# Performance work log

Hardware: AMD Instinct MI355X
Metric: run time of the kernel (lower is better)

## Reference

```python
import jax, jax.numpy as jnp
import numpy as np

NUM_HEADS = 8
OUTPUT_DIM = 64  # per-head dim
TEMP = float(OUTPUT_DIM ** 0.5)  # torch code: 1 / output_dim ** (-0.5) == sqrt(output_dim)


def setup_inputs() -> dict:
    key = jax.random.key(0)
    ks = jax.random.split(key, 5)
    B, N, Lq, S, D = 8, 4, 64, 1024, 1024
    inner = OUTPUT_DIM * NUM_HEADS  # 512
    scale = 0.02
    return {
        "q": jax.random.normal(ks[0], (B, N, Lq, D), dtype=jnp.float32),
        "k_v": jax.random.normal(ks[1], (B, N, S, D), dtype=jnp.float32),
        "W_kv": jax.random.normal(ks[2], (inner * 2, D), dtype=jnp.float32) * scale,
        "W_q": jax.random.normal(ks[3], (inner, D), dtype=jnp.float32) * scale,
        "W_out": jax.random.normal(ks[4], (D, inner), dtype=jnp.float32) * scale,
    }


def _split_heads(x):
    # b n s (h d) -> b n h s d
    b, n, s, hd = x.shape
    return x.reshape(b, n, s, NUM_HEADS, hd // NUM_HEADS).transpose(0, 1, 3, 2, 4)


def reference(q, k_v, W_kv, W_q, W_out):
    # Concatenate latents onto the key/value sequence (Perceiver resampler style)
    kv = jnp.concatenate([k_v, q], axis=-2)            # [b, n, S+Lq, D]
    k, v = jnp.split(kv @ W_kv.T, 2, axis=-1)          # each [b, n, S+Lq, h*d]
    qp = q @ W_q.T                                     # [b, n, Lq, h*d]
    qh = _split_heads(qp) * TEMP                       # NOTE: up-scaled by sqrt(d), as in source
    kh = _split_heads(k)
    vh = _split_heads(v)
    scores = jnp.einsum('bnhqd,bnhkd->bnhqk', qh, kh)
    attn = jax.nn.softmax(scores, axis=-1)
    o = jnp.einsum('bnhqk,bnhkd->bnhqd', attn, vh)
    b, n, h, s, d = o.shape
    o = o.transpose(0, 1, 3, 2, 4).reshape(b, n, s, h * d)  # b n h s d -> b n s (h d)
    return o @ W_out.T
```

## Files before the change

kernel.cpp:

```cpp
#include <hip/hip_runtime.h>
#include <math.h>


namespace {

typedef __attribute__((ext_vector_type(8))) short s16x8;
typedef __attribute__((ext_vector_type(4))) float f32x4;

constexpr int LDP = 68;
constexpr int LDB = 72;

constexpr size_t CWS_OFF  = 0;
constexpr size_t QP_OFF   = 142606336;
constexpr size_t WKVH_OFF = 146800640;
constexpr size_t WKVL_OFF = 148897792;
constexpr size_t WQH_OFF  = 150994944;
constexpr size_t WQL_OFF  = 152043520;
constexpr size_t WOH_OFF  = 153092096;
constexpr size_t WOL_OFF  = 154140672;
constexpr size_t OHI_OFF  = 155189248;
constexpr size_t OLO_OFF  = 157286400;
constexpr size_t WS_REQUIRED = 159383552;

__device__ __forceinline__ float4 ld4(const float* p) {
    return *reinterpret_cast<const float4*>(p);
}
__device__ __forceinline__ unsigned short f2bf(float x) {
    unsigned u = __float_as_uint(x);
    u += 0x7fffu + ((u >> 16) & 1u);
    return (unsigned short)(u >> 16);
}
__device__ __forceinline__ float bf2f(unsigned short h) {
    return __uint_as_float(((unsigned)h) << 16);
}
__device__ __forceinline__ f32x4 mfma16(s16x8 a, s16x8 b, f32x4 c) {
    return __builtin_amdgcn_mfma_f32_16x16x32_bf16(a, b, c, 0, 0, 0);
}

__device__ __forceinline__ void cvt_row(const float* __restrict__ src,
                                        unsigned short* __restrict__ dhi,
                                        unsigned short* __restrict__ dlo, int nelem) {
    const int t = threadIdx.x;
    if (t * 4 < nelem) {
        float4 v = ld4(src + t * 4);
        ushort4 hi, lo;
        hi.x = f2bf(v.x); lo.x = f2bf(v.x - bf2f(hi.x));
        hi.y = f2bf(v.y); lo.y = f2bf(v.y - bf2f(hi.y));
        hi.z = f2bf(v.z); lo.z = f2bf(v.z - bf2f(hi.z));
        hi.w = f2bf(v.w); lo.w = f2bf(v.w - bf2f(hi.w));
        *reinterpret_cast<ushort4*>(dhi + t * 4) = hi;
        *reinterpret_cast<ushort4*>(dlo + t * 4) = lo;
    }
}

__device__ __forceinline__ unsigned packbf(float x) {
    const unsigned short h = f2bf(x);
    return ((unsigned)h << 16) | (unsigned)f2bf(x - bf2f(h));
}

__global__ __launch_bounds__(256)
void cvt_b(float* __restrict__ kv, float* __restrict__ q,
           const float* __restrict__ Wkv, const float* __restrict__ Wq,
           const float* __restrict__ Wout,
           unsigned short* Wkvh, unsigned short* Wkvl,
           unsigned short* Wqh, unsigned short* Wql,
           unsigned short* Woh, unsigned short* Wol)
{
    const int b = blockIdx.x;
    const int t = threadIdx.x;
    if (b < 34816) {
        const int bn = b / 1088, s = b % 1088;
        float* row = (s < 1024) ? kv + ((size_t)bn * 1024 + s) * 1024
                                : q  + ((size_t)bn * 64 + (s - 1024)) * 1024;
        float4 v = ld4(row + t * 4);
        uint4 p;
        p.x = packbf(v.x); p.y = packbf(v.y);
        p.z = packbf(v.z); p.w = packbf(v.w);
        *reinterpret_cast<uint4*>(row + t * 4) = p;
    } else if (b < 34816 + 1024) {
        const int r = b - 34816;
        cvt_row(Wkv + (size_t)r * 1024, Wkvh + (size_t)r * 1024, Wkvl + (size_t)r * 1024, 1024);
    } else if (b < 34816 + 1536) {
        const int r = b - 34816 - 1024;
        cvt_row(Wq + (size_t)r * 1024, Wqh + (size_t)r * 1024, Wql + (size_t)r * 1024, 1024);
    } else {
        const int r = b - 34816 - 1536;
        cvt_row(Wout + (size_t)r * 512, Woh + (size_t)r * 512, Wol + (size_t)r * 512, 512);
    }
}

template<int CONCAT>
__global__ __launch_bounds__(256, 2)
void gemm_packed(const unsigned* __restrict__ Akv, const unsigned* __restrict__ Aq,
                 const unsigned short* __restrict__ Bhi, const unsigned short* __restrict__ Blo,
                 float* __restrict__ C, int N, int K, float scale)
{
    __shared__ short Ah[128][LDB], Al[128][LDB], Bh[128][LDB], Bl[128][LDB];

    const int bm   = blockIdx.y, bnn = blockIdx.x;
    const int tid  = threadIdx.x;
    const int lane = tid & 63, wave = tid >> 6;
    const int wr   = wave >> 1, wc = wave & 1;
    const int fr   = lane & 15, kg = lane >> 4;

    const unsigned* abase[8];
    int aprow[8], apcol[8];
    #pragma unroll
    for (int s2 = 0; s2 < 8; ++s2) {
        const int u = tid + 256 * s2;
        aprow[s2] = u >> 4;
        apcol[s2] = (u & 15) * 4;
        const int R = bm * 128 + aprow[s2];
        if (CONCAT) {
            const int bn = R / 1088, s = R - bn * 1088;
            abase[s2] = (s < 1024) ? Akv + ((size_t)bn * 1024 + s) * (size_t)K
                                   : Aq  + ((size_t)bn * 64 + (s - 1024)) * (size_t)K;
        } else {
            abase[s2] = Akv + (size_t)R * (size_t)K;
        }
    }
    int brow[4], bkk[4];
    #pragma unroll
    for (int s2 = 0; s2 < 4; ++s2) {
        const int u = tid + 256 * s2;
        brow[s2] = u >> 3;
        bkk[s2]  = (u & 7) * 8;
    }

    f32x4 acc[4][4] = {};

    for (int kc = 0; kc < K; kc += 64) {
        uint4 pa[8]; s16x8 wh[4], wl[4];
        #pragma unroll
        for (int s2 = 0; s2 < 8; ++s2)
            pa[s2] = *reinterpret_cast<const uint4*>(abase[s2] + kc + apcol[s2]);
        #pragma unroll
        for (int s2 = 0; s2 < 4; ++s2) {
            const size_t boff = (size_t)(bnn * 128 + brow[s2]) * (size_t)K + kc + bkk[s2];
            wh[s2] = *reinterpret_cast<const s16x8*>(Bhi + boff);
            wl[s2] = *reinterpret_cast<const s16x8*>(Blo + boff);
        }
        __syncthreads();
        #pragma unroll
        for (int s2 = 0; s2 < 8; ++s2) {
            ushort4 hi, lo;
            hi.x = (unsigned short)(pa[s2].x >> 16); lo.x = (unsigned short)(pa[s2].x & 0xffffu);
            hi.y = (unsigned short)(pa[s2].y >> 16); lo.y = (unsigned short)(pa[s2].y & 0xffffu);
            hi.z = (unsigned short)(pa[s2].z >> 16); lo.z = (unsigned short)(pa[s2].z & 0xffffu);
            hi.w = (unsigned short)(pa[s2].w >> 16); lo.w = (unsigned short)(pa[s2].w & 0xffffu);
            *reinterpret_cast<ushort4*>(&Ah[aprow[s2]][apcol[s2]]) = hi;
            *reinterpret_cast<ushort4*>(&Al[aprow[s2]][apcol[s2]]) = lo;
        }
        #pragma unroll
        for (int s2 = 0; s2 < 4; ++s2) {
            *reinterpret_cast<s16x8*>(&Bh[brow[s2]][bkk[s2]]) = wh[s2];
            *reinterpret_cast<s16x8*>(&Bl[brow[s2]][bkk[s2]]) = wl[s2];
        }
        __syncthreads();

        #pragma unroll
        for (int ks = 0; ks < 2; ++ks) {
            const int k0 = ks * 32 + kg * 8;
            s16x8 fah[4], fal[4], fbh[4], fbl[4];
            #pragma unroll
            for (int i = 0; i < 4; ++i) {
                fah[i] = *reinterpret_cast<const s16x8*>(&Ah[wr * 64 + i * 16 + fr][k0]);
                fal[i] = *reinterpret_cast<const s16x8*>(&Al[wr * 64 + i * 16 + fr][k0]);
            }
            #pragma unroll
            for (int j = 0; j < 4; ++j) {
                fbh[j] = *reinterpret_cast<const s16x8*>(&Bh[wc * 64 + j * 16 + fr][k0]);
                fbl[j] = *reinterpret_cast<const s16x8*>(&Bl[wc * 64 + j * 16 + fr][k0]);
            }
            #pragma unroll
            for (int i = 0; i < 4; ++i)
                #pragma unroll
                for (int j = 0; j < 4; ++j) {
                    acc[i][j] = mfma16(fah[i], fbh[j], acc[i][j]);
                    acc[i][j] = mfma16(fah[i], fbl[j], acc[i][j]);
                    acc[i][j] = mfma16(fal[i], fbh[j], acc[i][j]);
                }
        }
    }

    #pragma unroll
    for (int i = 0; i < 4; ++i)
        #pragma unroll
        for (int j = 0; j < 4; ++j) {
            const int row0 = bm * 128 + wr * 64 + i * 16 + kg * 4;
            const int col  = bnn * 128 + wc * 64 + j * 16 + fr;
            #pragma unroll
            for (int t = 0; t < 4; ++t)
                C[(size_t)(row0 + t) * N + col] = acc[i][j][t] * scale;
        }
}

__global__ __launch_bounds__(256, 2)
void gemm3(const unsigned short* __restrict__ Ahi, const unsigned short* __restrict__ Alo,
           const unsigned short* __restrict__ Bhi, const unsigned short* __restrict__ Blo,
           float* __restrict__ C, int N, int K, float scale)
{
    __shared__ short Ah[128][LDB], Al[128][LDB], Bh[128][LDB], Bl[128][LDB];

    const int bm   = blockIdx.y, bnn = blockIdx.x;
    const int tid  = threadIdx.x;
    const int lane = tid & 63, wave = tid >> 6;
    const int wr   = wave >> 1, wc = wave & 1;
    const int fr   = lane & 15, kg = lane >> 4;

    int srow[4], skk[4];
    #pragma unroll
    for (int s2 = 0; s2 < 4; ++s2) {
        const int u = tid + 256 * s2;
        srow[s2] = u >> 3;
        skk[s2]  = (u & 7) * 8;
    }

    f32x4 acc[4][4] = {};

    for (int kc = 0; kc < K; kc += 64) {
        s16x8 va[4], vb[4], vc[4], vd[4];
        #pragma unroll
        for (int s2 = 0; s2 < 4; ++s2) {
            const size_t aoff = (size_t)(bm * 128 + srow[s2]) * (size_t)K + kc + skk[s2];
            const size_t boff = (size_t)(bnn * 128 + srow[s2]) * (size_t)K + kc + skk[s2];
            va[s2] = *reinterpret_cast<const s16x8*>(Ahi + aoff);
            vb[s2] = *reinterpret_cast<const s16x8*>(Alo + aoff);
            vc[s2] = *reinterpret_cast<const s16x8*>(Bhi + boff);
            vd[s2] = *reinterpret_cast<const s16x8*>(Blo + boff);
        }
        __syncthreads();
        #pragma unroll
        for (int s2 = 0; s2 < 4; ++s2) {
            *reinterpret_cast<s16x8*>(&Ah[srow[s2]][skk[s2]]) = va[s2];
            *reinterpret_cast<s16x8*>(&Al[srow[s2]][skk[s2]]) = vb[s2];
            *reinterpret_cast<s16x8*>(&Bh[srow[s2]][skk[s2]]) = vc[s2];
            *reinterpret_cast<s16x8*>(&Bl[srow[s2]][skk[s2]]) = vd[s2];
        }
        __syncthreads();

        #pragma unroll
        for (int ks = 0; ks < 2; ++ks) {
            const int k0 = ks * 32 + kg * 8;
            s16x8 fah[4], fal[4], fbh[4], fbl[4];
            #pragma unroll
            for (int i = 0; i < 4; ++i) {
                fah[i] = *reinterpret_cast<const s16x8*>(&Ah[wr * 64 + i * 16 + fr][k0]);
                fal[i] = *reinterpret_cast<const s16x8*>(&Al[wr * 64 + i * 16 + fr][k0]);
            }
            #pragma unroll
            for (int j = 0; j < 4; ++j) {
                fbh[j] = *reinterpret_cast<const s16x8*>(&Bh[wc * 64 + j * 16 + fr][k0]);
                fbl[j] = *reinterpret_cast<const s16x8*>(&Bl[wc * 64 + j * 16 + fr][k0]);
            }
            #pragma unroll
            for (int i = 0; i < 4; ++i)
                #pragma unroll
                for (int j = 0; j < 4; ++j) {
                    acc[i][j] = mfma16(fah[i], fbh[j], acc[i][j]);
                    acc[i][j] = mfma16(fah[i], fbl[j], acc[i][j]);
                    acc[i][j] = mfma16(fal[i], fbh[j], acc[i][j]);
                }
        }
    }

    #pragma unroll
    for (int i = 0; i < 4; ++i)
        #pragma unroll
        for (int j = 0; j < 4; ++j) {
            const int row0 = bm * 128 + wr * 64 + i * 16 + kg * 4;
            const int col  = bnn * 128 + wc * 64 + j * 16 + fr;
            #pragma unroll
            for (int t = 0; t < 4; ++t)
                C[(size_t)(row0 + t) * N + col] = acc[i][j][t] * scale;
        }
}

__global__ __launch_bounds__(256, 1)
void attn2(const float* __restrict__ Qp, const float* __restrict__ Cws,
           unsigned short* __restrict__ Ohi, unsigned short* __restrict__ Olo)
{
    const int blk = blockIdx.x;
    const int bn = blk >> 3, h = blk & 7;
    const int tid = threadIdx.x;
    const int tx = tid & 15, ty = tid >> 4;

    __shared__ float Qs[64][LDP], Ks[64][LDP], Vs[64][LDP], Ps[64][LDP];

    #pragma unroll
    for (int i = 0; i < 4; ++i) {
        const int r = ty + 16 * i;
        *reinterpret_cast<float4*>(&Qs[r][tx * 4]) =
            ld4(Qp + (size_t)(bn * 64 + r) * 512 + h * 64 + tx * 4);
    }

    float O[4][4] = {};
    float m_run[4], l_run[4];
    #pragma unroll
    for (int i = 0; i < 4; ++i) { m_run[i] = -1e30f; l_run[i] = 0.0f; }

    for (int t = 0; t < 17; ++t) {
        __syncthreads();
        #pragma unroll
        for (int i = 0; i < 4; ++i) {
            const int r = ty + 16 * i;
            const size_t srow = (size_t)(bn * 1088 + t * 64 + r) * 1024;
            *reinterpret_cast<float4*>(&Ks[r][tx * 4]) = ld4(Cws + srow + h * 64 + tx * 4);
            *reinterpret_cast<float4*>(&Vs[r][tx * 4]) = ld4(Cws + srow + 512 + h * 64 + tx * 4);
        }
        __syncthreads();

        float sc[4][4] = {};
        #pragma unroll 4
        for (int k = 0; k < 64; k += 4) {
            float4 qa[4], kb[4];
            #pragma unroll
            for (int i = 0; i < 4; ++i) qa[i] = ld4(&Qs[ty * 4 + i][k]);
            #pragma unroll
            for (int j = 0; j < 4; ++j) kb[j] = ld4(&Ks[tx + 16 * j][k]);
            #pragma unroll
            for (int i = 0; i < 4; ++i)
                #pragma unroll
                for (int j = 0; j < 4; ++j)
                    sc[i][j] += qa[i].x * kb[j].x + qa[i].y * kb[j].y +
                                qa[i].z * kb[j].z + qa[i].w * kb[j].w;
        }

        #pragma unroll
        for (int i = 0; i < 4; ++i) {
            float mx = fmaxf(fmaxf(sc[i][0], sc[i][1]), fmaxf(sc[i][2], sc[i][3]));
            mx = fmaxf(mx, __shfl_xor(mx, 1, 16));
            mx = fmaxf(mx, __shfl_xor(mx, 2, 16));
            mx = fmaxf(mx, __shfl_xor(mx, 4, 16));
            mx = fmaxf(mx, __shfl_xor(mx, 8, 16));
            const float mnew  = fmaxf(m_run[i], mx);
            const float alpha = __expf(m_run[i] - mnew);
            float psum = 0.0f;
            #pragma unroll
            for (int j = 0; j < 4; ++j) {
                const float p = __expf(sc[i][j] - mnew);
                Ps[ty * 4 + i][tx + 16 * j] = p;
                psum += p;
            }
            psum += __shfl_xor(psum, 1, 16);
            psum += __shfl_xor(psum, 2, 16);
            psum += __shfl_xor(psum, 4, 16);
            psum += __shfl_xor(psum, 8, 16);
            l_run[i] = l_run[i] * alpha + psum;
            m_run[i] = mnew;
            #pragma unroll
            for (int j = 0; j < 4; ++j) O[i][j] *= alpha;
        }
        __syncthreads();

        #pragma unroll 4
        for (int s = 0; s < 64; s += 4) {
            float4 pa[4], vb[4];
            #pragma unroll
            for (int i = 0; i < 4; ++i) pa[i] = ld4(&Ps[ty * 4 + i][s]);
            #pragma unroll
            for (int m = 0; m < 4; ++m) vb[m] = ld4(&Vs[s + m][tx * 4]);
            #pragma unroll
            for (int i = 0; i < 4; ++i) {
                O[i][0] += pa[i].x * vb[0].x + pa[i].y * vb[1].x + pa[i].z * vb[2].x + pa[i].w * vb[3].x;
                O[i][1] += pa[i].x * vb[0].y + pa[i].y * vb[1].y + pa[i].z * vb[2].y + pa[i].w * vb[3].y;
                O[i][2] += pa[i].x * vb[0].z + pa[i].y * vb[1].z + pa[i].z * vb[2].z + pa[i].w * vb[3].z;
                O[i][3] += pa[i].x * vb[0].w + pa[i].y * vb[1].w + pa[i].z * vb[2].w + pa[i].w * vb[3].w;
            }
        }
    }

    #pragma unroll
    for (int i = 0; i < 4; ++i) {
        const float inv = 1.0f / l_run[i];
        const float v0 = O[i][0] * inv, v1 = O[i][1] * inv,
                    v2 = O[i][2] * inv, v3 = O[i][3] * inv;
        ushort4 hi, lo;
        hi.x = f2bf(v0); lo.x = f2bf(v0 - bf2f(hi.x));
        hi.y = f2bf(v1); lo.y = f2bf(v1 - bf2f(hi.y));
        hi.z = f2bf(v2); lo.z = f2bf(v2 - bf2f(hi.z));
        hi.w = f2bf(v3); lo.w = f2bf(v3 - bf2f(hi.w));
        const size_t idx = (size_t)(bn * 64 + ty * 4 + i) * 512 + h * 64 + tx * 4;
        *reinterpret_cast<ushort4*>(Ohi + idx) = hi;
        *reinterpret_cast<ushort4*>(Olo + idx) = lo;
    }
}

__global__ __launch_bounds__(256, 1)
void fused_attn(const float* __restrict__ q, const float* __restrict__ kv,
                const float* __restrict__ Wkv, const float* __restrict__ Wq,
                float* __restrict__ o_ws)
{
    const int blk = blockIdx.x;
    const int bn  = blk >> 3;
    const int h   = blk & 7;
    const int tid = threadIdx.x;
    const int tx  = tid & 15;
    const int ty  = tid >> 4;

    __shared__ float Qs[64][LDP];
    __shared__ float Ks[64][LDP];
    __shared__ float Vs[64][LDP];
    __shared__ float Ps[64][LDP];
    __shared__ float Xs[64][LDP];
    __shared__ float Ws[128][LDP];

    const float* qbn = q + (size_t)bn * 64 * 1024;

    {
        const float* Wqh = Wq + (size_t)(h * 64) * 1024;
        float acc[4][4] = {};
        for (int kc = 0; kc < 1024; kc += 64) {
            __syncthreads();
            #pragma unroll
            for (int kk = 0; kk < 4; ++kk) {
                const int r = ty + 16 * kk;
                *reinterpret_cast<float4*>(&Xs[r][tx * 4]) = ld4(qbn + (size_t)r * 1024 + kc + tx * 4);
                *reinterpret_cast<float4*>(&Ws[r][tx * 4]) = ld4(Wqh + (size_t)r * 1024 + kc + tx * 4);
            }
            __syncthreads();
            #pragma unroll 4
            for (int k = 0; k < 64; k += 4) {
                float4 xa[4], wb[4];
                #pragma unroll
                for (int i = 0; i < 4; ++i) xa[i] = ld4(&Xs[ty * 4 + i][k]);
                #pragma unroll
                for (int j = 0; j < 4; ++j) wb[j] = ld4(&Ws[tx + 16 * j][k]);
                #pragma unroll
                for (int i = 0; i < 4; ++i)
                    #pragma unroll
                    for (int j = 0; j < 4; ++j)
                        acc[i][j] += xa[i].x * wb[j].x + xa[i].y * wb[j].y +
                                     xa[i].z * wb[j].z + xa[i].w * wb[j].w;
            }
        }
        #pragma unroll
        for (int i = 0; i < 4; ++i)
            #pragma unroll
            for (int j = 0; j < 4; ++j)
                Qs[ty * 4 + i][tx + 16 * j] = 8.0f * acc[i][j];
    }

    float O[4][4] = {};
    float m_run[4], l_run[4];
    #pragma unroll
    for (int i = 0; i < 4; ++i) { m_run[i] = -1e30f; l_run[i] = 0.0f; }

    for (int t = 0; t < 17; ++t) {
        const float* Xsrc = (t < 16) ? (kv + ((size_t)bn * 1024 + (size_t)t * 64) * 1024) : qbn;

        float acc2[4][8] = {};
        float4 px[4], pw[8];
        {
            #pragma unroll
            for (int kk = 0; kk < 4; ++kk)
                px[kk] = ld4(Xsrc + (size_t)(ty + 16 * kk) * 1024 + tx * 4);
            #pragma unroll
            for (int kk = 0; kk < 8; ++kk) {
                const int r = ty + 16 * kk;
                const int wrow = (kk < 4) ? (h * 64 + r) : (448 + h * 64 + r);
                pw[kk] = ld4(Wkv + (size_t)wrow * 1024 + tx * 4);
            }
        }
        for (int c = 0; c < 16; ++c) {
            __syncthreads();
            #pragma unroll
            for (int kk = 0; kk < 4; ++kk)
                *reinterpret_cast<float4*>(&Xs[ty + 16 * kk][tx * 4]) = px[kk];
            #pragma unroll
            for (int kk = 0; kk < 8; ++kk)
                *reinterpret_cast<float4*>(&Ws[ty + 16 * kk][tx * 4]) = pw[kk];
            __syncthreads();
            if (c < 15) {
                const int kc = (c + 1) * 64;
                #pragma unroll
                for (int kk = 0; kk < 4; ++kk)
                    px[kk] = ld4(Xsrc + (size_t)(ty + 16 * kk) * 1024 + kc + tx * 4);
                #pragma unroll
                for (int kk = 0; kk < 8; ++kk) {
                    const int r = ty + 16 * kk;
                    const int wrow = (kk < 4) ? (h * 64 + r) : (448 + h * 64 + r);
                    pw[kk] = ld4(Wkv + (size_t)wrow * 1024 + kc + tx * 4);
                }
            }
            #pragma unroll 4
            for (int k = 0; k < 64; k += 4) {
                float4 xa[4], wb[8];
                #pragma unroll
                for (int i = 0; i < 4; ++i) xa[i] = ld4(&Xs[ty * 4 + i][k]);
                #pragma unroll
                for (int j = 0; j < 8; ++j) wb[j] = ld4(&Ws[tx + 16 * j][k]);
                #pragma unroll
                for (int i = 0; i < 4; ++i)
                    #pragma unroll
                    for (int j = 0; j < 8; ++j)
                        acc2[i][j] += xa[i].x * wb[j].x + xa[i].y * wb[j].y +
                                      xa[i].z * wb[j].z + xa[i].w * wb[j].w;
            }
        }
        #pragma unroll
        for (int i = 0; i < 4; ++i) {
            #pragma unroll
            for (int j = 0; j < 4; ++j) Ks[ty * 4 + i][tx + 16 * j] = acc2[i][j];
            #pragma unroll
            for (int j = 0; j < 4; ++j) Vs[ty * 4 + i][tx + 16 * j] = acc2[i][4 + j];
        }
        __syncthreads();

        float sc[4][4] = {};
        #pragma unroll 4
        for (int k = 0; k < 64; k += 4) {
            float4 qa[4], kb[4];
            #pragma unroll
            for (int i = 0; i < 4; ++i) qa[i] = ld4(&Qs[ty * 4 + i][k]);
            #pragma unroll
            for (int j = 0; j < 4; ++j) kb[j] = ld4(&Ks[tx + 16 * j][k]);
            #pragma unroll
            for (int i = 0; i < 4; ++i)
                #pragma unroll
                for (int j = 0; j < 4; ++j)
                    sc[i][j] += qa[i].x * kb[j].x + qa[i].y * kb[j].y +
                                qa[i].z * kb[j].z + qa[i].w * kb[j].w;
        }

        #pragma unroll
        for (int i = 0; i < 4; ++i) {
            float mx = fmaxf(fmaxf(sc[i][0], sc[i][1]), fmaxf(sc[i][2], sc[i][3]));
            mx = fmaxf(mx, __shfl_xor(mx, 1, 16));
            mx = fmaxf(mx, __shfl_xor(mx, 2, 16));
            mx = fmaxf(mx, __shfl_xor(mx, 4, 16));
            mx = fmaxf(mx, __shfl_xor(mx, 8, 16));
            const float mnew  = fmaxf(m_run[i], mx);
            const float alpha = __expf(m_run[i] - mnew);
            float psum = 0.0f;
            #pragma unroll
            for (int j = 0; j < 4; ++j) {
                const float p = __expf(sc[i][j] - mnew);
                Ps[ty * 4 + i][tx + 16 * j] = p;
                psum += p;
            }
            psum += __shfl_xor(psum, 1, 16);
            psum += __shfl_xor(psum, 2, 16);
            psum += __shfl_xor(psum, 4, 16);
            psum += __shfl_xor(psum, 8, 16);
            l_run[i] = l_run[i] * alpha + psum;
            m_run[i] = mnew;
            #pragma unroll
            for (int j = 0; j < 4; ++j) O[i][j] *= alpha;
        }
        __syncthreads();

        #pragma unroll 4
        for (int s = 0; s < 64; s += 4) {
            float4 pa[4], vb[4];
            #pragma unroll
            for (int i = 0; i < 4; ++i) pa[i] = ld4(&Ps[ty * 4 + i][s]);
            #pragma unroll
            for (int m = 0; m < 4; ++m) vb[m] = ld4(&Vs[s + m][tx * 4]);
            #pragma unroll
            for (int i = 0; i < 4; ++i) {
                O[i][0] += pa[i].x * vb[0].x + pa[i].y * vb[1].x + pa[i].z * vb[2].x + pa[i].w * vb[3].x;
                O[i][1] += pa[i].x * vb[0].y + pa[i].y * vb[1].y + pa[i].z * vb[2].y + pa[i].w * vb[3].y;
                O[i][2] += pa[i].x * vb[0].z + pa[i].y * vb[1].z + pa[i].z * vb[2].z + pa[i].w * vb[3].z;
                O[i][3] += pa[i].x * vb[0].w + pa[i].y * vb[1].w + pa[i].z * vb[2].w + pa[i].w * vb[3].w;
            }
        }
    }

    #pragma unroll
    for (int i = 0; i < 4; ++i) {
        const float inv = 1.0f / l_run[i];
        float4 r;
        r.x = O[i][0] * inv; r.y = O[i][1] * inv;
        r.z = O[i][2] * inv; r.w = O[i][3] * inv;
        *reinterpret_cast<float4*>(
            &o_ws[((size_t)bn * 64 + ty * 4 + i) * 512 + h * 64 + tx * 4]) = r;
    }
}

__global__ __launch_bounds__(256, 1)
void out_proj(const float* __restrict__ A, const float* __restrict__ W,
              float* __restrict__ out)
{
    const int bm  = blockIdx.y;
    const int bnc = blockIdx.x;
    const int tid = threadIdx.x;
    const int tx  = tid & 15;
    const int ty  = tid >> 4;

    __shared__ float As[64][LDP];
    __shared__ float Bs[64][LDP];

    float acc[4][4] = {};
    const float* Ab = A + (size_t)bm * 64 * 512;
    const float* Wb = W + (size_t)bnc * 64 * 512;

    for (int kc = 0; kc < 512; kc += 64) {
        __syncthreads();
        #pragma unroll
        for (int kk = 0; kk < 4; ++kk) {
            const int r = ty + 16 * kk;
            *reinterpret_cast<float4*>(&As[r][tx * 4]) = ld4(Ab + (size_t)r * 512 + kc + tx * 4);
            *reinterpret_cast<float4*>(&Bs[r][tx * 4]) = ld4(Wb + (size_t)r * 512 + kc + tx * 4);
        }
        __syncthreads();
        #pragma unroll 4
        for (int k = 0; k < 64; k += 4) {
            float4 xa[4], wb[4];
            #pragma unroll
            for (int i = 0; i < 4; ++i) xa[i] = ld4(&As[ty * 4 + i][k]);
            #pragma unroll
            for (int j = 0; j < 4; ++j) wb[j] = ld4(&Bs[tx + 16 * j][k]);
            #pragma unroll
            for (int i = 0; i < 4; ++i)
                #pragma unroll
                for (int j = 0; j < 4; ++j)
                    acc[i][j] += xa[i].x * wb[j].x + xa[i].y * wb[j].y +
                                 xa[i].z * wb[j].z + xa[i].w * wb[j].w;
        }
    }
    #pragma unroll
    for (int i = 0; i < 4; ++i)
        #pragma unroll
        for (int j = 0; j < 4; ++j)
            out[((size_t)bm * 64 + ty * 4 + i) * 1024 + bnc * 64 + tx + 16 * j] = acc[i][j];
}

}

extern "C" void kernel_launch(void* const* d_in, const int* in_sizes, int n_in,
                              void* d_out, int out_size, void* d_ws, size_t ws_size,
                              hipStream_t stream)
{
    (void)in_sizes; (void)n_in; (void)out_size;
    float* q    = (float*)d_in[0];
    float* kv   = (float*)d_in[1];
    const float* Wkv  = (const float*)d_in[2];
    const float* Wq   = (const float*)d_in[3];
    const float* Wout = (const float*)d_in[4];
    float* out = (float*)d_out;
    char*  ws  = (char*)d_ws;

    if (ws_size >= WS_REQUIRED) {
        float*          Cws  = (float*)(ws + CWS_OFF);
        float*          Qp   = (float*)(ws + QP_OFF);
        unsigned short* Wkvh = (unsigned short*)(ws + WKVH_OFF);
        unsigned short* Wkvl = (unsigned short*)(ws + WKVL_OFF);
        unsigned short* Wqh  = (unsigned short*)(ws + WQH_OFF);
        unsigned short* Wql  = (unsigned short*)(ws + WQL_OFF);
        unsigned short* Woh  = (unsigned short*)(ws + WOH_OFF);
        unsigned short* Wol  = (unsigned short*)(ws + WOL_OFF);
        unsigned short* Ohi  = (unsigned short*)(ws + OHI_OFF);
        unsigned short* Olo  = (unsigned short*)(ws + OLO_OFF);

        hipLaunchKernelGGL(cvt_b, dim3(37376), dim3(256), 0, stream,
                           kv, q, Wkv, Wq, Wout,
                           Wkvh, Wkvl, Wqh, Wql, Woh, Wol);
        hipLaunchKernelGGL((gemm_packed<1>), dim3(8, 272), dim3(256), 0, stream,
                           (const unsigned*)kv, (const unsigned*)q,
                           Wkvh, Wkvl, Cws, 1024, 1024, 1.0f);
        hipLaunchKernelGGL((gemm_packed<0>), dim3(4, 16), dim3(256), 0, stream,
                           (const unsigned*)q, (const unsigned*)q,
                           Wqh, Wql, Qp, 512, 1024, 8.0f);
        hipLaunchKernelGGL(attn2, dim3(256), dim3(256), 0, stream,
                           Qp, Cws, Ohi, Olo);
        hipLaunchKernelGGL(gemm3, dim3(8, 16), dim3(256), 0, stream,
                           Ohi, Olo, Woh, Wol, out, 1024, 512, 1.0f);
    } else {
        float* o_ws = (float*)d_ws;
        hipLaunchKernelGGL(fused_attn, dim3(256), dim3(256), 0, stream,
                           q, kv, Wkv, Wq, o_ws);
        hipLaunchKernelGGL(out_proj, dim3(16, 32), dim3(256), 0, stream,
                           o_ws, Wout, out);
    }
}
```

Before: 606.4 us.

## Drop low-bf16 correction terms for V projection and output GEMM, add XCD swizzle

The KV projection GEMM now runs the 3-term split-bf16 product only for the K half of the columns, and a single bf16 MFMA for the V half. The output projection becomes a plain one-term bf16 GEMM fed by hi-only attention output and hi-only W_out. This removes the lo-part conversions, their loads and stores, and two thirds of the MFMAs on those paths. Separately, the GEMM grid is flattened and remapped with an XCD-aware swizzle for better L2 locality. The cost is lower precision on V and on the final projection, which may push error toward the tolerance.

```diff
diff --git a/kernel.cpp b/kernel.cpp
--- a/kernel.cpp
+++ b/kernel.cpp
@@ -17,9 +17,7 @@
 constexpr size_t WQH_OFF  = 150994944;
 constexpr size_t WQL_OFF  = 152043520;
 constexpr size_t WOH_OFF  = 153092096;
-constexpr size_t WOL_OFF  = 154140672;
 constexpr size_t OHI_OFF  = 155189248;
-constexpr size_t OLO_OFF  = 157286400;
 constexpr size_t WS_REQUIRED = 159383552;
 
 __device__ __forceinline__ float4 ld4(const float* p) {
@@ -35,6 +33,11 @@
 }
 __device__ __forceinline__ f32x4 mfma16(s16x8 a, s16x8 b, f32x4 c) {
     return __builtin_amdgcn_mfma_f32_16x16x32_bf16(a, b, c, 0, 0, 0);
+}
+__device__ __forceinline__ int xcd_swizzle(int fid, int nwg) {
+    const int xcd = fid & 7, off = fid >> 3;
+    const int q = nwg >> 3, r = nwg & 7;
+    return (xcd < r ? xcd * (q + 1) : r * (q + 1) + (xcd - r) * q) + off;
 }
 
 __device__ __forceinline__ void cvt_row(const float* __restrict__ src,
@@ -52,6 +55,16 @@
         *reinterpret_cast<ushort4*>(dlo + t * 4) = lo;
     }
 }
+__device__ __forceinline__ void cvt_row_hi(const float* __restrict__ src,
+                                           unsigned short* __restrict__ dhi, int nelem) {
+    const int t = threadIdx.x;
+    if (t * 4 < nelem) {
+        float4 v = ld4(src + t * 4);
+        ushort4 hi;
+        hi.x = f2bf(v.x); hi.y = f2bf(v.y); hi.z = f2bf(v.z); hi.w = f2bf(v.w);
+        *reinterpret_cast<ushort4*>(dhi + t * 4) = hi;
+    }
+}
 
 __device__ __forceinline__ unsigned packbf(float x) {
     const unsigned short h = f2bf(x);
@@ -64,7 +77,7 @@
            const float* __restrict__ Wout,
            unsigned short* Wkvh, unsigned short* Wkvl,
            unsigned short* Wqh, unsigned short* Wql,
-           unsigned short* Woh, unsigned short* Wol)
+           unsigned short* Woh)
 {
     const int b = blockIdx.x;
     const int t = threadIdx.x;
@@ -85,19 +98,21 @@
         cvt_row(Wq + (size_t)r * 1024, Wqh + (size_t)r * 1024, Wql + (size_t)r * 1024, 1024);
     } else {
         const int r = b - 34816 - 1536;
-        cvt_row(Wout + (size_t)r * 512, Woh + (size_t)r * 512, Wol + (size_t)r * 512, 512);
-    }
-}
-
-template<int CONCAT>
+        cvt_row_hi(Wout + (size_t)r * 512, Woh + (size_t)r * 512, 512);
+    }
+}
+
+template<int CONCAT, int NCOL>
 __global__ __launch_bounds__(256, 2)
 void gemm_packed(const unsigned* __restrict__ Akv, const unsigned* __restrict__ Aq,
                  const unsigned short* __restrict__ Bhi, const unsigned short* __restrict__ Blo,
-                 float* __restrict__ C, int N, int K, float scale)
+                 float* __restrict__ C, int N, int K, float scale, int split_col)
 {
     __shared__ short Ah[128][LDB], Al[128][LDB], Bh[128][LDB], Bl[128][LDB];
 
-    const int bm   = blockIdx.y, bnn = blockIdx.x;
+    const int w    = xcd_swizzle(blockIdx.x, gridDim.x);
+    const int bm   = w / NCOL, bnn = w % NCOL;
+    const int terms3 = (bnn * 128 < split_col);
     const int tid  = threadIdx.x;
     const int lane = tid & 63, wave = tid >> 6;
     const int wr   = wave >> 1, wc = wave & 1;
@@ -138,48 +153,84 @@
         for (int s2 = 0; s2 < 4; ++s2) {
             const size_t boff = (size_t)(bnn * 128 + brow[s2]) * (size_t)K + kc + bkk[s2];
             wh[s2] = *reinterpret_cast<const s16x8*>(Bhi + boff);
-            wl[s2] = *reinterpret_cast<const s16x8*>(Blo + boff);
+        }
+        if (terms3) {
+            #pragma unroll
+            for (int s2 = 0; s2 < 4; ++s2) {
+                const size_t boff = (size_t)(bnn * 128 + brow[s2]) * (size_t)K + kc + bkk[s2];
+                wl[s2] = *reinterpret_cast<const s16x8*>(Blo + boff);
+            }
         }
         __syncthreads();
         #pragma unroll
         for (int s2 = 0; s2 < 8; ++s2) {
-            ushort4 hi, lo;
-            hi.x = (unsigned short)(pa[s2].x >> 16); lo.x = (unsigned short)(pa[s2].x & 0xffffu);
-            hi.y = (unsigned short)(pa[s2].y >> 16); lo.y = (unsigned short)(pa[s2].y & 0xffffu);
-            hi.z = (unsigned short)(pa[s2].z >> 16); lo.z = (unsigned short)(pa[s2].z & 0xffffu);
-            hi.w = (unsigned short)(pa[s2].w >> 16); lo.w = (unsigned short)(pa[s2].w & 0xffffu);
+            ushort4 hi;
+            hi.x = (unsigned short)(pa[s2].x >> 16);
+            hi.y = (unsigned short)(pa[s2].y >> 16);
+            hi.z = (unsigned short)(pa[s2].z >> 16);
+            hi.w = (unsigned short)(pa[s2].w >> 16);
             *reinterpret_cast<ushort4*>(&Ah[aprow[s2]][apcol[s2]]) = hi;
-            *reinterpret_cast<ushort4*>(&Al[aprow[s2]][apcol[s2]]) = lo;
-        }
-        #pragma unroll
-        for (int s2 = 0; s2 < 4; ++s2) {
+        }
+        #pragma unroll
+        for (int s2 = 0; s2 < 4; ++s2)
             *reinterpret_cast<s16x8*>(&Bh[brow[s2]][bkk[s2]]) = wh[s2];
-            *reinterpret_cast<s16x8*>(&Bl[brow[s2]][bkk[s2]]) = wl[s2];
-        }
-        __syncthreads();
-
-        #pragma unroll
-        for (int ks = 0; ks < 2; ++ks) {
-            const int k0 = ks * 32 + kg * 8;
-            s16x8 fah[4], fal[4], fbh[4], fbl[4];
-            #pragma unroll
-            for (int i = 0; i < 4; ++i) {
-                fah[i] = *reinterpret_cast<const s16x8*>(&Ah[wr * 64 + i * 16 + fr][k0]);
-                fal[i] = *reinterpret_cast<const s16x8*>(&Al[wr * 64 + i * 16 + fr][k0]);
-            }
-            #pragma unroll
-            for (int j = 0; j < 4; ++j) {
-                fbh[j] = *reinterpret_cast<const s16x8*>(&Bh[wc * 64 + j * 16 + fr][k0]);
-                fbl[j] = *reinterpret_cast<const s16x8*>(&Bl[wc * 64 + j * 16 + fr][k0]);
-            }
-            #pragma unroll
-            for (int i = 0; i < 4; ++i)
+        if (terms3) {
+            #pragma unroll
+            for (int s2 = 0; s2 < 8; ++s2) {
+                ushort4 lo;
+                lo.x = (unsigned short)(pa[s2].x & 0xffffu);
+                lo.y = (unsigned short)(pa[s2].y & 0xffffu);
+                lo.z = (unsigned short)(pa[s2].z & 0xffffu);
+                lo.w = (unsigned short)(pa[s2].w & 0xffffu);
+                *reinterpret_cast<ushort4*>(&Al[aprow[s2]][apcol[s2]]) = lo;
+            }
+            #pragma unroll
+            for (int s2 = 0; s2 < 4; ++s2)
+                *reinterpret_cast<s16x8*>(&Bl[brow[s2]][bkk[s2]]) = wl[s2];
+        }
+        __syncthreads();
+
+        if (terms3) {
+            #pragma unroll
+            for (int ks = 0; ks < 2; ++ks) {
+                const int k0 = ks * 32 + kg * 8;
+                s16x8 fah[4], fal[4], fbh[4], fbl[4];
+                #pragma unroll
+                for (int i = 0; i < 4; ++i) {
+                    fah[i] = *reinterpret_cast<const s16x8*>(&Ah[wr * 64 + i * 16 + fr][k0]);
+                    fal[i] = *reinterpret_cast<const s16x8*>(&Al[wr * 64 + i * 16 + fr][k0]);
+                }
                 #pragma unroll
                 for (int j = 0; j < 4; ++j) {
-                    acc[i][j] = mfma16(fah[i], fbh[j], acc[i][j]);
-                    acc[i][j] = mfma16(fah[i], fbl[j], acc[i][j]);
-                    acc[i][j] = mfma16(fal[i], fbh[j], acc[i][j]);
+                    fbh[j] = *reinterpret_cast<const s16x8*>(&Bh[wc * 64 + j * 16 + fr][k0]);
+                    fbl[j] = *reinterpret_cast<const s16x8*>(&Bl[wc * 64 + j * 16 + fr][k0]);
                 }
+                #pragma unroll
+                for (int i = 0; i < 4; ++i)
+                    #pragma unroll
+                    for (int j = 0; j < 4; ++j) {
+                        acc[i][j] = mfma16(fah[i], fbh[j], acc[i][j]);
+                        acc[i][j] = mfma16(fah[i], fbl[j], acc[i][j]);
+                        acc[i][j] = mfma16(fal[i], fbh[j], acc[i][j]);
+                    }
+            }
+        } else {
+            #pragma unroll
+            for (int ks = 0; ks < 2; ++ks) {
+                const int k0 = ks * 32 + kg * 8;
+                s16x8 fah[4], fbh[4];
+                #pragma unroll
+                for (int i = 0; i < 4; ++i)
+                    fah[i] = *reinterpret_cast<const s16x8*>(&Ah[wr * 64 + i * 16 + fr][k0]);
+                #pragma unroll
+                for (int j = 0; j < 4; ++j)
+                    fbh[j] = *reinterpret_cast<const s16x8*>(&Bh[wc * 64 + j * 16 + fr][k0]);
+                #pragma unroll
+                for (int i = 0; i < 4; ++i)
+                    #pragma unroll
+                    for (int j = 0; j < 4; ++j)
+                        acc[i][j] = mfma16(fah[i], fbh[j], acc[i][j]);
+            }
         }
     }
 
@@ -195,12 +246,11 @@
         }
 }
 
-__global__ __launch_bounds__(256, 2)
-void gemm3(const unsigned short* __restrict__ Ahi, const unsigned short* __restrict__ Alo,
-           const unsigned short* __restrict__ Bhi, const unsigned short* __restrict__ Blo,
-           float* __restrict__ C, int N, int K, float scale)
+__global__ __launch_bounds__(256, 4)
+void gemm1(const unsigned short* __restrict__ Ahi, const unsigned short* __restrict__ Bhi,
+           float* __restrict__ C, int N, int K)
 {
-    __shared__ short Ah[128][LDB], Al[128][LDB], Bh[128][LDB], Bl[128][LDB];
+    __shared__ short Ah[128][LDB], Bh[128][LDB];
 
     const int bm   = blockIdx.y, bnn = blockIdx.x;
     const int tid  = threadIdx.x;
@@ -219,48 +269,37 @@
     f32x4 acc[4][4] = {};
 
     for (int kc = 0; kc < K; kc += 64) {
-        s16x8 va[4], vb[4], vc[4], vd[4];
+        s16x8 va[4], vc[4];
         #pragma unroll
         for (int s2 = 0; s2 < 4; ++s2) {
             const size_t aoff = (size_t)(bm * 128 + srow[s2]) * (size_t)K + kc + skk[s2];
             const size_t boff = (size_t)(bnn * 128 + srow[s2]) * (size_t)K + kc + skk[s2];
             va[s2] = *reinterpret_cast<const s16x8*>(Ahi + aoff);
-            vb[s2] = *reinterpret_cast<const s16x8*>(Alo + aoff);
             vc[s2] = *reinterpret_cast<const s16x8*>(Bhi + boff);
-            vd[s2] = *reinterpret_cast<const s16x8*>(Blo + boff);
         }
         __syncthreads();
         #pragma unroll
         for (int s2 = 0; s2 < 4; ++s2) {
             *reinterpret_cast<s16x8*>(&Ah[srow[s2]][skk[s2]]) = va[s2];
-            *reinterpret_cast<s16x8*>(&Al[srow[s2]][skk[s2]]) = vb[s2];
             *reinterpret_cast<s16x8*>(&Bh[srow[s2]][skk[s2]]) = vc[s2];
-            *reinterpret_cast<s16x8*>(&Bl[srow[s2]][skk[s2]]) = vd[s2];
         }
         __syncthreads();
 
         #pragma unroll
         for (int ks = 0; ks < 2; ++ks) {
             const int k0 = ks * 32 + kg * 8;
-            s16x8 fah[4], fal[4], fbh[4], fbl[4];
-            #pragma unroll
-            for (int i = 0; i < 4; ++i) {
+            s16x8 fah[4], fbh[4];
+            #pragma unroll
+            for (int i = 0; i < 4; ++i)
                 fah[i] = *reinterpret_cast<const s16x8*>(&Ah[wr * 64 + i * 16 + fr][k0]);
-                fal[i] = *reinterpret_cast<const s16x8*>(&Al[wr * 64 + i * 16 + fr][k0]);
-            }
-            #pragma unroll
-            for (int j = 0; j < 4; ++j) {
+            #pragma unroll
+            for (int j = 0; j < 4; ++j)
                 fbh[j] = *reinterpret_cast<const s16x8*>(&Bh[wc * 64 + j * 16 + fr][k0]);
-                fbl[j] = *reinterpret_cast<const s16x8*>(&Bl[wc * 64 + j * 16 + fr][k0]);
-            }
             #pragma unroll
             for (int i = 0; i < 4; ++i)
                 #pragma unroll
-                for (int j = 0; j < 4; ++j) {
+                for (int j = 0; j < 4; ++j)
                     acc[i][j] = mfma16(fah[i], fbh[j], acc[i][j]);
-                    acc[i][j] = mfma16(fah[i], fbl[j], acc[i][j]);
-                    acc[i][j] = mfma16(fal[i], fbh[j], acc[i][j]);
-                }
         }
     }
 
@@ -272,13 +311,13 @@
             const int col  = bnn * 128 + wc * 64 + j * 16 + fr;
             #pragma unroll
             for (int t = 0; t < 4; ++t)
-                C[(size_t)(row0 + t) * N + col] = acc[i][j][t] * scale;
+                C[(size_t)(row0 + t) * N + col] = acc[i][j][t];
         }
 }
 
 __global__ __launch_bounds__(256, 1)
 void attn2(const float* __restrict__ Qp, const float* __restrict__ Cws,
-           unsigned short* __restrict__ Ohi, unsigned short* __restrict__ Olo)
+           unsigned short* __restrict__ Ohi)
 {
     const int blk = blockIdx.x;
     const int bn = blk >> 3, h = blk & 7;
@@ -373,16 +412,13 @@
     #pragma unroll
     for (int i = 0; i < 4; ++i) {
         const float inv = 1.0f / l_run[i];
-        const float v0 = O[i][0] * inv, v1 = O[i][1] * inv,
-                    v2 = O[i][2] * inv, v3 = O[i][3] * inv;
-        ushort4 hi, lo;
-        hi.x = f2bf(v0); lo.x = f2bf(v0 - bf2f(hi.x));
-        hi.y = f2bf(v1); lo.y = f2bf(v1 - bf2f(hi.y));
-        hi.z = f2bf(v2); lo.z = f2bf(v2 - bf2f(hi.z));
-        hi.w = f2bf(v3); lo.w = f2bf(v3 - bf2f(hi.w));
+        ushort4 hi;
+        hi.x = f2bf(O[i][0] * inv);
+        hi.y = f2bf(O[i][1] * inv);
+        hi.z = f2bf(O[i][2] * inv);
+        hi.w = f2bf(O[i][3] * inv);
         const size_t idx = (size_t)(bn * 64 + ty * 4 + i) * 512 + h * 64 + tx * 4;
         *reinterpret_cast<ushort4*>(Ohi + idx) = hi;
-        *reinterpret_cast<ushort4*>(Olo + idx) = lo;
     }
 }
 
@@ -649,23 +685,21 @@
         unsigned short* Wqh  = (unsigned short*)(ws + WQH_OFF);
         unsigned short* Wql  = (unsigned short*)(ws + WQL_OFF);
         unsigned short* Woh  = (unsigned short*)(ws + WOH_OFF);
-        unsigned short* Wol  = (unsigned short*)(ws + WOL_OFF);
         unsigned short* Ohi  = (unsigned short*)(ws + OHI_OFF);
-        unsigned short* Olo  = (unsigned short*)(ws + OLO_OFF);
 
         hipLaunchKernelGGL(cvt_b, dim3(37376), dim3(256), 0, stream,
                            kv, q, Wkv, Wq, Wout,
-                           Wkvh, Wkvl, Wqh, Wql, Woh, Wol);
-        hipLaunchKernelGGL((gemm_packed<1>), dim3(8, 272), dim3(256), 0, stream,
+                           Wkvh, Wkvl, Wqh, Wql, Woh);
+        hipLaunchKernelGGL((gemm_packed<1, 8>), dim3(2176), dim3(256), 0, stream,
                            (const unsigned*)kv, (const unsigned*)q,
-                           Wkvh, Wkvl, Cws, 1024, 1024, 1.0f);
-        hipLaunchKernelGGL((gemm_packed<0>), dim3(4, 16), dim3(256), 0, stream,
+                           Wkvh, Wkvl, Cws, 1024, 1024, 1.0f, 512);
+        hipLaunchKernelGGL((gemm_packed<0, 4>), dim3(64), dim3(256), 0, stream,
                            (const unsigned*)q, (const unsigned*)q,
-                           Wqh, Wql, Qp, 512, 1024, 8.0f);
+                           Wqh, Wql, Qp, 512, 1024, 8.0f, 1 << 30);
         hipLaunchKernelGGL(attn2, dim3(256), dim3(256), 0, stream,
-                           Qp, Cws, Ohi, Olo);
-        hipLaunchKernelGGL(gemm3, dim3(8, 16), dim3(256), 0, stream,
-                           Ohi, Olo, Woh, Wol, out, 1024, 512, 1.0f);
+                           Qp, Cws, Ohi);
+        hipLaunchKernelGGL(gemm1, dim3(8, 16), dim3(256), 0, stream,
+                           Ohi, Woh, out, 1024, 512);
     } else {
         float* o_ws = (float*)d_ws;
         hipLaunchKernelGGL(fused_attn, dim3(256), dim3(256), 0, stream,
```

Measured after the change: 690.4 us. +13.8%, slower.
